# Kernel tuning notes

Measured on AMD Instinct MI355X. Metric: run time of the kernel, lower is better.

The kernel has to match this reference:

```python
import jax, jax.numpy as jnp
import numpy as np

NUM_GROUPS = 32
EPS = 1e-6
HEAD = 8


def group_norm(x, gamma, beta):
    # x: (b, c, h, w); normalize per group of channels over (c/g, h, w)
    b, c, h, w = x.shape
    g = NUM_GROUPS
    xg = x.reshape(b, g, c // g, h, w)
    mean = xg.mean(axis=(2, 3, 4), keepdims=True)
    var = xg.var(axis=(2, 3, 4), keepdims=True)
    xn = ((xg - mean) * jax.lax.rsqrt(var + EPS)).reshape(b, c, h, w)
    return xn * gamma[None, :, None, None] + beta[None, :, None, None]


def setup_inputs() -> dict:
    key = jax.random.key(0)
    ks = jax.random.split(key, 6)
    b, c, h, w = 8, 512, 64, 64
    sd = 1.0 / np.sqrt(c)
    return {
        "x": jax.random.normal(ks[0], (b, c, h, w), jnp.float32),
        "gamma": jnp.ones((c,), jnp.float32),
        "beta": jnp.zeros((c,), jnp.float32),
        "Wq": jax.random.normal(ks[1], (c, c), jnp.float32) * sd,
        "Wk": jax.random.normal(ks[2], (c, c), jnp.float32) * sd,
        "Wv": jax.random.normal(ks[3], (c, c), jnp.float32) * sd,
        "Wp": jax.random.normal(ks[4], (c, c), jnp.float32) * sd,
        "bp": jnp.zeros((c,), jnp.float32),
    }


def reference(x, gamma, beta, Wq, Wk, Wv, Wp, bp):
    b, c, h, w = x.shape
    hd = c // HEAD
    scale = jnp.sqrt(jnp.float32(hd))  # NOTE: original MULTIPLIES by sqrt(d)
    xn = group_norm(x, gamma, beta)            # (b, c, h, w)
    x_ = xn.reshape(b, c, h * w).transpose(0, 2, 1)  # (b, n, c), n = h*w
    # torch Linear: y = x @ W.T
    Q = (x_ @ Wq.T).reshape(b, h * w, HEAD, hd)
    K = (x_ @ Wk.T).reshape(b, h * w, HEAD, hd)
    V = (x_ @ Wv.T).reshape(b, h * w, HEAD, hd)
    # einsum 'bhid,bhjd->bhij' with axes (b, n, head, hd): per-position head gram
    dots = jnp.einsum('bnid,bnjd->bnij', Q, K) * scale  # (b, n, head, head)
    att = jax.nn.softmax(dots, axis=1)  # softmax over the SPATIAL axis (dim=1)
    out = jnp.einsum('bnij,bnjd->bnid', att, V).reshape(b, h * w, c)
    out = out @ Wp.T + bp  # dropout is identity at inference
    return out.transpose(0, 2, 1).reshape(b, c, h, w) + xn  # residual adds normed x
```

## Files before the change

kernel.cpp:

```cpp
#include <hip/hip_runtime.h>
#include <stdint.h>

typedef unsigned short ushort_t;
typedef _Float16 half8 __attribute__((ext_vector_type(8)));
typedef float f32x4 __attribute__((ext_vector_type(4)));

#define GLOBAL_AS __attribute__((address_space(1)))
#define LDS_AS    __attribute__((address_space(3)))

__device__ __forceinline__ float bf2f(ushort_t u) {
    union { unsigned i; float f; } v; v.i = ((unsigned)u) << 16; return v.f;
}
__device__ __forceinline__ ushort_t f2h(float f) {
    union { _Float16 h; ushort_t u; } v; v.h = (_Float16)f; return v.u;
}
__device__ __forceinline__ float h2f(ushort_t u) {
    union { _Float16 h; ushort_t u; } v; v.u = u; return (float)v.h;
}

__device__ __forceinline__ void async16(const void* g, void* l) {
    __builtin_amdgcn_global_load_lds((const GLOBAL_AS uint32_t*)g,
                                     (LDS_AS uint32_t*)l, 16, 0, 0);
}

__device__ __forceinline__ int is_bf16_in(const uint32_t* g32) {
    return *g32 == 0x3F803F80u;
}

__global__ __launch_bounds__(256) void prep(const void* Wq, const void* Wk,
                                            const void* Wv, const void* Wp,
                                            const void* g, const void* be, const void* bp,
                                            ushort_t* Wh, float* gcan, float* bcan,
                                            float* bpcan, const uint32_t* g32) {
    const int id = blockIdx.x;
    const int isbf = is_bf16_in(g32);
    if (id < 512) {
        const int wsel = id >> 7, wblk = id & 127;
        const void* src = (wsel == 0) ? Wq : (wsel == 1) ? Wk : (wsel == 2) ? Wv : Wp;
        ushort_t* dst = Wh + (size_t)wsel * 262144;
        const int e0 = wblk * 2048 + threadIdx.x * 8;
        ushort_t o[8];
        if (isbf) {
            uint4 u = *(const uint4*)((const ushort_t*)src + e0);
            const ushort_t* e = (const ushort_t*)&u;
#pragma unroll
            for (int j = 0; j < 8; ++j) o[j] = f2h(bf2f(e[j]));
        } else {
            float4 a = *(const float4*)((const float*)src + e0);
            float4 b = *(const float4*)((const float*)src + e0 + 4);
            o[0] = f2h(a.x); o[1] = f2h(a.y); o[2] = f2h(a.z); o[3] = f2h(a.w);
            o[4] = f2h(b.x); o[5] = f2h(b.y); o[6] = f2h(b.z); o[7] = f2h(b.w);
        }
        *(uint4*)(dst + e0) = *(const uint4*)o;
    } else {
        int t = threadIdx.x + (id - 512) * 256;
        if (isbf) {
            gcan[t]  = bf2f(((const ushort_t*)g)[t]);
            bcan[t]  = bf2f(((const ushort_t*)be)[t]);
            bpcan[t] = bf2f(((const ushort_t*)bp)[t]);
        } else {
            gcan[t]  = ((const float*)g)[t];
            bcan[t]  = ((const float*)be)[t];
            bpcan[t] = ((const float*)bp)[t];
        }
    }
}

__global__ __launch_bounds__(256) void gn_part(const void* xv, float* __restrict__ psums,
                                               const uint32_t* g32) {
    const int bx = blockIdx.x, t = threadIdx.x;
    const size_t base = (size_t)(bx >> 3) * 65536 + (size_t)(bx & 7) * 8192;
    float s = 0.f, sq = 0.f;
    if (is_bf16_in(g32)) {
        const ushort_t* p = (const ushort_t*)xv + base;
        for (int i = 0; i < 4; ++i) {
            uint4 u = ((const uint4*)p)[t + 256 * i];
            const ushort_t* e = (const ushort_t*)&u;
#pragma unroll
            for (int j = 0; j < 8; ++j) { float f = bf2f(e[j]); s += f; sq += f * f; }
        }
    } else {
        const float* p = (const float*)xv + base;
        for (int i = 0; i < 8; ++i) {
            float4 v = ((const float4*)p)[t + 256 * i];
            s += v.x + v.y + v.z + v.w;
            sq += v.x * v.x + v.y * v.y + v.z * v.z + v.w * v.w;
        }
    }
    __shared__ float ls[256], lq[256];
    ls[t] = s; lq[t] = sq;
    __syncthreads();
    for (int off = 128; off > 0; off >>= 1) {
        if (t < off) { ls[t] += ls[t + off]; lq[t] += lq[t + off]; }
        __syncthreads();
    }
    if (t == 0) { psums[bx * 2] = ls[0]; psums[bx * 2 + 1] = lq[0]; }
}

__global__ __launch_bounds__(256) void gn_apply_t(const void* xv,
                                                  const float* __restrict__ gcan,
                                                  const float* __restrict__ bcan,
                                                  const float* __restrict__ psums,
                                                  ushort_t* __restrict__ xnt,
                                                  ushort_t* __restrict__ xnc,
                                                  const uint32_t* g32) {
    const int nt = blockIdx.x;
    const int ct = blockIdx.y;
    const int b  = blockIdx.z;
    const int t  = threadIdx.x;
    const int c0 = ct * 64, n0 = nt * 64;
    __shared__ __align__(16) ushort_t tile[64 * 80];
    __shared__ float scS[64], shS[64];
    if (t < 64) {
        int c = c0 + t;
        int g = c >> 4;
        float s = 0.f, q = 0.f;
#pragma unroll
        for (int k = 0; k < 8; ++k) {
            s += psums[((b * 32 + g) * 8 + k) * 2];
            q += psums[((b * 32 + g) * 8 + k) * 2 + 1];
        }
        float mean = s * (1.f / 65536.f);
        float var  = q * (1.f / 65536.f) - mean * mean;
        float rstd = rsqrtf(fmaxf(var, 0.f) + 1e-6f);
        float sc = rstd * gcan[c];
        scS[t] = sc;
        shS[t] = bcan[c] - mean * sc;
    }
    __syncthreads();
    if (is_bf16_in(g32)) {
        const ushort_t* x = (const ushort_t*)xv;
#pragma unroll
        for (int p = 0; p < 2; ++p) {
            int u = p * 256 + t;
            int cc = u >> 3, nc = u & 7;
            int c = c0 + cc;
            size_t gidx = ((size_t)(b * 512 + c)) * 4096 + n0 + nc * 8;
            uint4 raw = *(const uint4*)(x + gidx);
            float sc = scS[cc], sh = shS[cc];
            const ushort_t* e = (const ushort_t*)&raw;
            ushort_t hv[8];
#pragma unroll
            for (int j = 0; j < 8; ++j) {
                hv[j] = f2h(bf2f(e[j]) * sc + sh);
                tile[(nc * 8 + j) * 80 + cc] = hv[j];
            }
            *(uint4*)(xnc + gidx) = *(const uint4*)hv;
        }
    } else {
        const float* x = (const float*)xv;
#pragma unroll
        for (int p = 0; p < 4; ++p) {
            int u = p * 256 + t;
            int cc = u >> 4, nc = u & 15;
            int c = c0 + cc;
            size_t gidx = ((size_t)(b * 512 + c)) * 4096 + n0 + nc * 4;
            float4 raw = *(const float4*)(x + gidx);
            float sc = scS[cc], sh = shS[cc];
            ushort_t hv[4];
            hv[0] = f2h(raw.x * sc + sh);
            hv[1] = f2h(raw.y * sc + sh);
            hv[2] = f2h(raw.z * sc + sh);
            hv[3] = f2h(raw.w * sc + sh);
#pragma unroll
            for (int j = 0; j < 4; ++j) tile[(nc * 4 + j) * 80 + cc] = hv[j];
            *(uint2*)(xnc + gidx) = *(const uint2*)hv;
        }
    }
    __syncthreads();
#pragma unroll
    for (int p = 0; p < 2; ++p) {
        int u = p * 256 + t;
        int nn = u >> 3, cchunk = u & 7;
        uint4 o = *(const uint4*)(tile + nn * 80 + cchunk * 8);
        *(uint4*)(xnt + ((size_t)(b * 4096 + n0 + nn)) * 512 + c0 + cchunk * 8) = o;
    }
}

__device__ __forceinline__ void gemm128_core(const ushort_t* __restrict__ A,
                                             const ushort_t* __restrict__ B,
                                             int m0, int n0, int K, f32x4 acc[4][4]) {
    __shared__ __align__(16) ushort_t As[128 * 32];
    __shared__ __align__(16) ushort_t Bs[128 * 32];
    const int t = threadIdx.x;
    const int l = t & 63;
    const int w = t >> 6;
    const int wm = (w >> 1) * 64, wn = (w & 1) * 64;
    const int lr = l & 15, q = l >> 4;
    f32x4 zero = {0.f, 0.f, 0.f, 0.f};
#pragma unroll
    for (int mi = 0; mi < 4; ++mi)
#pragma unroll
        for (int ni = 0; ni < 4; ++ni) acc[mi][ni] = zero;

    for (int kt = 0; kt < K; kt += 32) {
        __syncthreads();
#pragma unroll
        for (int p = 0; p < 2; ++p) {
            int s = p * 256 + t;
            int r = s >> 2, kc = s & 3;
            async16(A + (size_t)(m0 + r) * K + kt + kc * 8, (char*)As + p * 4096 + w * 1024);
            async16(B + (size_t)(n0 + r) * K + kt + kc * 8, (char*)Bs + p * 4096 + w * 1024);
        }
        __syncthreads();
        half8 af[4], bf[4];
#pragma unroll
        for (int mi = 0; mi < 4; ++mi)
            af[mi] = *(const half8*)(As + (wm + mi * 16 + lr) * 32 + q * 8);
#pragma unroll
        for (int ni = 0; ni < 4; ++ni)
            bf[ni] = *(const half8*)(Bs + (wn + ni * 16 + lr) * 32 + q * 8);
#pragma unroll
        for (int mi = 0; mi < 4; ++mi)
#pragma unroll
            for (int ni = 0; ni < 4; ++ni)
                acc[mi][ni] = __builtin_amdgcn_mfma_f32_16x16x32_f16(af[mi], bf[ni],
                                                                    acc[mi][ni], 0, 0, 0);
    }
}

__global__ __launch_bounds__(256) void gemm_qkv(const ushort_t* __restrict__ xnt,
                                                const ushort_t* __restrict__ Wh,
                                                ushort_t* __restrict__ Qo,
                                                ushort_t* __restrict__ Ko,
                                                ushort_t* __restrict__ Vo) {
    const int id = blockIdx.x;
    const int xcd = id & 7, s = id >> 3;
    const int mloc = s / 12, r = s % 12;
    const int m0 = (xcd * 32 + mloc) * 128;
    const int n0 = (r & 3) * 128;
    const int z  = r >> 2;
    const ushort_t* B = Wh + (size_t)z * 262144;
    ushort_t* C = (z == 0) ? Qo : (z == 1) ? Ko : Vo;
    f32x4 acc[4][4];
    gemm128_core(xnt, B, m0, n0, 512, acc);
    const int t = threadIdx.x, l = t & 63, w = t >> 6;
    const int wm = (w >> 1) * 64, wn = (w & 1) * 64;
    const int col = l & 15, q = l >> 4;
#pragma unroll
    for (int mi = 0; mi < 4; ++mi)
#pragma unroll
        for (int ni = 0; ni < 4; ++ni)
#pragma unroll
            for (int rr = 0; rr < 4; ++rr) {
                int row = wm + mi * 16 + q * 4 + rr;
                int cc  = wn + ni * 16 + col;
                C[(size_t)(m0 + row) * 512 + n0 + cc] = f2h(acc[mi][ni][rr]);
            }
}

__global__ __launch_bounds__(256) void dots_smax(const ushort_t* __restrict__ Q,
                                                 const ushort_t* __restrict__ K,
                                                 float* __restrict__ dots,
                                                 float* __restrict__ pmax,
                                                 float* __restrict__ psum) {
    const int chunk = blockIdx.x;
    const int t = threadIdx.x, l = t & 63, w = t >> 6;
    const int m = l & 15, q = l >> 4, col = m;
    __shared__ float sd[128][64];
    __shared__ float lm[4][64], lsum[4][64];
#pragma unroll
    for (int i = 0; i < 16; ++i) {
        int gpl = (i * 4 + w) * 2;
        int gp0 = chunk * 128 + gpl;
        const size_t base = (size_t)(gp0 + (m >> 3)) * 512 + (m & 7) * 64 + q * 8;
        half8 a0 = *(const half8*)(Q + base);
        half8 a1 = *(const half8*)(Q + base + 32);
        half8 b0 = *(const half8*)(K + base);
        half8 b1 = *(const half8*)(K + base + 32);
        f32x4 acc = {0.f, 0.f, 0.f, 0.f};
        acc = __builtin_amdgcn_mfma_f32_16x16x32_f16(a0, b0, acc, 0, 0, 0);
        acc = __builtin_amdgcn_mfma_f32_16x16x32_f16(a1, b1, acc, 0, 0, 0);
#pragma unroll
        for (int r = 0; r < 4; ++r) {
            int row = q * 4 + r;
            if (row < 8 && col < 8) {
                float v = acc[r] * 8.0f;
                int ij = row * 8 + col;
                sd[gpl][ij] = v;
                dots[(size_t)(gp0)*64 + ij] = v;
            }
            if (row >= 8 && col >= 8) {
                float v = acc[r] * 8.0f;
                int ij = (row - 8) * 8 + (col - 8);
                sd[gpl + 1][ij] = v;
                dots[(size_t)(gp0 + 1) * 64 + ij] = v;
            }
        }
    }
    __syncthreads();
    const int ij = l;
    float mx = -1e30f;
    float v[32];
#pragma unroll
    for (int r = 0; r < 32; ++r) { v[r] = sd[w * 32 + r][ij]; mx = fmaxf(mx, v[r]); }
    lm[w][ij] = mx;
    __syncthreads();
    float cm = fmaxf(fmaxf(lm[0][ij], lm[1][ij]), fmaxf(lm[2][ij], lm[3][ij]));
    float sum = 0.f;
#pragma unroll
    for (int r = 0; r < 32; ++r) sum += __expf(v[r] - cm);
    lsum[w][ij] = sum;
    __syncthreads();
    if (w == 0) {
        pmax[chunk * 64 + ij] = cm;
        psum[chunk * 64 + ij] = lsum[0][ij] + lsum[1][ij] + lsum[2][ij] + lsum[3][ij];
    }
}

__global__ __launch_bounds__(256) void attn_apply(const float* __restrict__ dots,
                                                  const float* __restrict__ pmax,
                                                  const float* __restrict__ psum,
                                                  const ushort_t* __restrict__ V,
                                                  ushort_t* __restrict__ P) {
    const int t = threadIdx.x, l = t & 63, w = t >> 6;
    const int gp_base = blockIdx.x * 16;
    const int b = gp_base >> 12;
    __shared__ float pm4[4][64], ps4[4][64];
    __shared__ float Mv[64], Siv[64];
    {
        const int cg = w * 8;
        float m = -1e30f;
        float pmv[8], psv[8];
#pragma unroll
        for (int c = 0; c < 8; ++c) {
            pmv[c] = pmax[(b * 32 + cg + c) * 64 + l];
            psv[c] = psum[(b * 32 + cg + c) * 64 + l];
            m = fmaxf(m, pmv[c]);
        }
        float s = 0.f;
#pragma unroll
        for (int c = 0; c < 8; ++c) s += psv[c] * __expf(pmv[c] - m);
        pm4[w][l] = m; ps4[w][l] = s;
    }
    __syncthreads();
    if (w == 0) {
        float M = fmaxf(fmaxf(pm4[0][l], pm4[1][l]), fmaxf(pm4[2][l], pm4[3][l]));
        float S = ps4[0][l] * __expf(pm4[0][l] - M) + ps4[1][l] * __expf(pm4[1][l] - M)
                + ps4[2][l] * __expf(pm4[2][l] - M) + ps4[3][l] * __expf(pm4[3][l] - M);
        Mv[l] = M;
        Siv[l] = 1.f / S;
    }
    __syncthreads();
    const float mv = Mv[l], siv = Siv[l];
    __shared__ float att[4][64];
    __shared__ __align__(16) ushort_t vb[4][512];
    const int i = l >> 3, dc = l & 7;
    for (int p = 0; p < 4; ++p) {
        int gp = gp_base + w * 4 + p;
        float d = dots[(size_t)gp * 64 + l];
        att[w][l] = __expf(d - mv) * siv;
        *(uint4*)(&vb[w][l * 8]) = *(const uint4*)(V + (size_t)gp * 512 + l * 8);
        __syncthreads();
        float o[8] = {0, 0, 0, 0, 0, 0, 0, 0};
#pragma unroll
        for (int j = 0; j < 8; ++j) {
            float a = att[w][i * 8 + j];
            uint4 vv = *(const uint4*)(&vb[w][j * 64 + dc * 8]);
            const ushort_t* ve = (const ushort_t*)&vv;
#pragma unroll
            for (int k2 = 0; k2 < 8; ++k2) o[k2] += a * h2f(ve[k2]);
        }
        ushort_t ou[8];
#pragma unroll
        for (int k2 = 0; k2 < 8; ++k2) ou[k2] = f2h(o[k2]);
        *(uint4*)(P + (size_t)gp * 512 + l * 8) = *(const uint4*)ou;
        __syncthreads();
    }
}

__global__ __launch_bounds__(256) void gemm_out(const ushort_t* __restrict__ Wph,
                                                const ushort_t* __restrict__ P,
                                                const ushort_t* __restrict__ xnc,
                                                const float* __restrict__ bpcan,
                                                float* __restrict__ out) {
    const int id = blockIdx.x;
    const int xcd = id & 7, s = id >> 3;
    const int pair = xcd * 32 + (s >> 2);
    const int o0 = (s & 3) * 128;
    const int b  = pair >> 5;
    const int n0 = (pair & 31) * 128;
    f32x4 acc[4][4];
    gemm128_core(Wph, P + (size_t)b * 4096 * 512, o0, n0, 512, acc);
    const int t = threadIdx.x, l = t & 63, w = t >> 6;
    const int wm = (w >> 1) * 64, wn = (w & 1) * 64;
    const int col = l & 15, q = l >> 4;
#pragma unroll
    for (int mi = 0; mi < 4; ++mi) {
#pragma unroll
        for (int r = 0; r < 4; ++r) {
            int o = o0 + wm + mi * 16 + q * 4 + r;
            float bias = bpcan[o];
#pragma unroll
            for (int ni = 0; ni < 4; ++ni) {
                int n = n0 + wn + ni * 16 + col;
                size_t idx = ((size_t)(b * 512 + o)) * 4096 + n;
                out[idx] = acc[mi][ni][r] + bias + h2f(xnc[idx]);
            }
        }
    }
}

extern "C" void kernel_launch(void* const* d_in, const int* in_sizes, int n_in,
                              void* d_out, int out_size, void* d_ws, size_t ws_size,
                              hipStream_t stream) {
    const void* x     = d_in[0];
    const void* gamma = d_in[1];
    const void* beta  = d_in[2];
    const void* Wq    = d_in[3];
    const void* Wk    = d_in[4];
    const void* Wv    = d_in[5];
    const void* Wp    = d_in[6];
    const void* bp    = d_in[7];
    const uint32_t* g32 = (const uint32_t*)gamma;
    float* out = (float*)d_out;

    char* ws = (char*)d_ws;
    const size_t SZ = 33554432;
    ushort_t* xnt = (ushort_t*)(ws);
    ushort_t* Qh  = (ushort_t*)(ws + 1 * SZ);
    ushort_t* Kh  = (ushort_t*)(ws + 2 * SZ);
    ushort_t* Vh  = (ushort_t*)(ws + 3 * SZ);
    float* dots   = (float*)(ws + 4 * SZ);
    ushort_t* Wh  = (ushort_t*)(ws + 4 * SZ + 8388608);
    ushort_t* xnc = (ushort_t*)(ws + 4 * SZ + 8388608 + 2097152);
    char* tail    = ws + 4 * SZ + 8388608 + 2097152 + SZ;
    float* gcan   = (float*)(tail);
    float* bcan   = gcan + 512;
    float* bpcan  = bcan + 512;
    float* psums  = bpcan + 512;
    float* pmax   = psums + 4096;
    float* psumS  = pmax + 16384;
    ushort_t* Pb  = xnt;

    prep      <<<514, 256, 0, stream>>>(Wq, Wk, Wv, Wp, gamma, beta, bp,
                                        Wh, gcan, bcan, bpcan, g32);
    gn_part   <<<2048, 256, 0, stream>>>(x, psums, g32);
    gn_apply_t<<<dim3(64, 8, 8), 256, 0, stream>>>(x, gcan, bcan, psums, xnt, xnc, g32);
    gemm_qkv  <<<3072, 256, 0, stream>>>(xnt, Wh, Qh, Kh, Vh);
    dots_smax <<<256, 256, 0, stream>>>(Qh, Kh, dots, pmax, psumS);
    attn_apply<<<2048, 256, 0, stream>>>(dots, pmax, psumS, Vh, Pb);
    gemm_out  <<<1024, 256, 0, stream>>>(Wh + 3 * 262144, Pb, xnc, bpcan, out);
}
```

Measured before the change: 288.2 us.

## Double-buffer GEMM LDS tiles with XOR swizzle and drop per-wave barriers

```diff
diff --git a/kernel.cpp b/kernel.cpp
--- a/kernel.cpp
+++ b/kernel.cpp
@@ -177,46 +177,69 @@
     }
 }
 
+__device__ __forceinline__ void mfma_tile(const ushort_t* Ab, const ushort_t* Bb,
+                                          int wm, int wn, int lr, int qe,
+                                          f32x4 acc[4][4]) {
+    half8 af[4], bf[4];
+#pragma unroll
+    for (int mi = 0; mi < 4; ++mi)
+        af[mi] = *(const half8*)(Ab + (wm + mi * 16 + lr) * 32 + qe * 8);
+#pragma unroll
+    for (int ni = 0; ni < 4; ++ni)
+        bf[ni] = *(const half8*)(Bb + (wn + ni * 16 + lr) * 32 + qe * 8);
+#pragma unroll
+    for (int mi = 0; mi < 4; ++mi)
+#pragma unroll
+        for (int ni = 0; ni < 4; ++ni)
+            acc[mi][ni] = __builtin_amdgcn_mfma_f32_16x16x32_f16(af[mi], bf[ni],
+                                                                 acc[mi][ni], 0, 0, 0);
+}
+
 __device__ __forceinline__ void gemm128_core(const ushort_t* __restrict__ A,
                                              const ushort_t* __restrict__ B,
                                              int m0, int n0, int K, f32x4 acc[4][4]) {
-    __shared__ __align__(16) ushort_t As[128 * 32];
-    __shared__ __align__(16) ushort_t Bs[128 * 32];
+    __shared__ __align__(16) ushort_t As[2][128 * 32];
+    __shared__ __align__(16) ushort_t Bs[2][128 * 32];
     const int t = threadIdx.x;
     const int l = t & 63;
     const int w = t >> 6;
     const int wm = (w >> 1) * 64, wn = (w & 1) * 64;
     const int lr = l & 15, q = l >> 4;
+    const int qe = q ^ ((lr >> 1) & 3);
+    const int r0 = t >> 2;
+    const int kc = (t & 3) ^ ((r0 >> 1) & 3);
+    const ushort_t* gA0 = A + (size_t)(m0 + r0) * K + kc * 8;
+    const ushort_t* gB0 = B + (size_t)(n0 + r0) * K + kc * 8;
+    const ushort_t* gA1 = gA0 + (size_t)64 * K;
+    const ushort_t* gB1 = gB0 + (size_t)64 * K;
+
     f32x4 zero = {0.f, 0.f, 0.f, 0.f};
 #pragma unroll
     for (int mi = 0; mi < 4; ++mi)
 #pragma unroll
         for (int ni = 0; ni < 4; ++ni) acc[mi][ni] = zero;
 
-    for (int kt = 0; kt < K; kt += 32) {
-        __syncthreads();
-#pragma unroll
-        for (int p = 0; p < 2; ++p) {
-            int s = p * 256 + t;
-            int r = s >> 2, kc = s & 3;
-            async16(A + (size_t)(m0 + r) * K + kt + kc * 8, (char*)As + p * 4096 + w * 1024);
-            async16(B + (size_t)(n0 + r) * K + kt + kc * 8, (char*)Bs + p * 4096 + w * 1024);
-        }
-        __syncthreads();
-        half8 af[4], bf[4];
-#pragma unroll
-        for (int mi = 0; mi < 4; ++mi)
-            af[mi] = *(const half8*)(As + (wm + mi * 16 + lr) * 32 + q * 8);
-#pragma unroll
-        for (int ni = 0; ni < 4; ++ni)
-            bf[ni] = *(const half8*)(Bs + (wn + ni * 16 + lr) * 32 + q * 8);
-#pragma unroll
-        for (int mi = 0; mi < 4; ++mi)
-#pragma unroll
-            for (int ni = 0; ni < 4; ++ni)
-                acc[mi][ni] = __builtin_amdgcn_mfma_f32_16x16x32_f16(af[mi], bf[ni],
-                                                                    acc[mi][ni], 0, 0, 0);
-    }
+    {
+        char* sA = (char*)&As[0][0] + w * 1024;
+        char* sB = (char*)&Bs[0][0] + w * 1024;
+        async16(gA0, sA); async16(gA1, sA + 4096);
+        async16(gB0, sB); async16(gB1, sB + 4096);
+    }
+    asm volatile("s_waitcnt vmcnt(0)" ::: "memory");
+    __builtin_amdgcn_s_barrier();
+
+    int cur = 0;
+    for (int kt = 32; kt < K; kt += 32) {
+        char* sA = (char*)&As[cur ^ 1][0] + w * 1024;
+        char* sB = (char*)&Bs[cur ^ 1][0] + w * 1024;
+        async16(gA0 + kt, sA); async16(gA1 + kt, sA + 4096);
+        async16(gB0 + kt, sB); async16(gB1 + kt, sB + 4096);
+        mfma_tile(&As[cur][0], &Bs[cur][0], wm, wn, lr, qe, acc);
+        asm volatile("s_waitcnt vmcnt(0)" ::: "memory");
+        __builtin_amdgcn_s_barrier();
+        cur ^= 1;
+    }
+    mfma_tile(&As[cur][0], &Bs[cur][0], wm, wn, lr, qe, acc);
 }
 
 __global__ __launch_bounds__(256) void gemm_qkv(const ushort_t* __restrict__ xnt,
@@ -351,7 +374,6 @@
         float d = dots[(size_t)gp * 64 + l];
         att[w][l] = __expf(d - mv) * siv;
         *(uint4*)(&vb[w][l * 8]) = *(const uint4*)(V + (size_t)gp * 512 + l * 8);
-        __syncthreads();
         float o[8] = {0, 0, 0, 0, 0, 0, 0, 0};
 #pragma unroll
         for (int j = 0; j < 8; ++j) {
@@ -365,7 +387,6 @@
 #pragma unroll
         for (int k2 = 0; k2 < 8; ++k2) ou[k2] = f2h(o[k2]);
         *(uint4*)(P + (size_t)gp * 512 + l * 8) = *(const uint4*)ou;
-        __syncthreads();
     }
 }
 
```

After: 309.2 us. 7.3% more time.

## Replace 128-tile GEMM core with double-buffered swizzled 256x256 tile pipeline

Applied to the files above, without the earlier changes.

```diff
diff --git a/kernel.cpp b/kernel.cpp
--- a/kernel.cpp
+++ b/kernel.cpp
@@ -177,75 +177,112 @@
     }
 }
 
-__device__ __forceinline__ void gemm128_core(const ushort_t* __restrict__ A,
-                                             const ushort_t* __restrict__ B,
-                                             int m0, int n0, int K, f32x4 acc[4][4]) {
-    __shared__ __align__(16) ushort_t As[128 * 32];
-    __shared__ __align__(16) ushort_t Bs[128 * 32];
+__device__ __forceinline__ void gemm256_core(const ushort_t* __restrict__ A,
+                                             const ushort_t* __restrict__ Bm,
+                                             int m0, int n0, f32x4 acc[8][4]) {
+    __shared__ __align__(16) ushort_t lds[2][4][8192];
     const int t = threadIdx.x;
-    const int l = t & 63;
-    const int w = t >> 6;
-    const int wm = (w >> 1) * 64, wn = (w & 1) * 64;
+    const int l = t & 63, w = t >> 6;
+    const int wmi = w >> 2, wni = w & 3;
     const int lr = l & 15, q = l >> 4;
+    const int rxor = lr & 7;
+    const int sr = t >> 3;
+    const int sc = (t & 7) ^ (sr & 7);
+
     f32x4 zero = {0.f, 0.f, 0.f, 0.f};
 #pragma unroll
-    for (int mi = 0; mi < 4; ++mi)
-#pragma unroll
-        for (int ni = 0; ni < 4; ++ni) acc[mi][ni] = zero;
-
-    for (int kt = 0; kt < K; kt += 32) {
-        __syncthreads();
-#pragma unroll
-        for (int p = 0; p < 2; ++p) {
-            int s = p * 256 + t;
-            int r = s >> 2, kc = s & 3;
-            async16(A + (size_t)(m0 + r) * K + kt + kc * 8, (char*)As + p * 4096 + w * 1024);
-            async16(B + (size_t)(n0 + r) * K + kt + kc * 8, (char*)Bs + p * 4096 + w * 1024);
-        }
-        __syncthreads();
-        half8 af[4], bf[4];
-#pragma unroll
-        for (int mi = 0; mi < 4; ++mi)
-            af[mi] = *(const half8*)(As + (wm + mi * 16 + lr) * 32 + q * 8);
-#pragma unroll
-        for (int ni = 0; ni < 4; ++ni)
-            bf[ni] = *(const half8*)(Bs + (wn + ni * 16 + lr) * 32 + q * 8);
-#pragma unroll
-        for (int mi = 0; mi < 4; ++mi)
-#pragma unroll
-            for (int ni = 0; ni < 4; ++ni)
-                acc[mi][ni] = __builtin_amdgcn_mfma_f32_16x16x32_f16(af[mi], bf[ni],
-                                                                    acc[mi][ni], 0, 0, 0);
-    }
-}
-
-__global__ __launch_bounds__(256) void gemm_qkv(const ushort_t* __restrict__ xnt,
-                                                const ushort_t* __restrict__ Wh,
-                                                ushort_t* __restrict__ Qo,
-                                                ushort_t* __restrict__ Ko,
-                                                ushort_t* __restrict__ Vo) {
+    for (int mf = 0; mf < 8; ++mf)
+#pragma unroll
+        for (int nf = 0; nf < 4; ++nf) acc[mf][nf] = zero;
+
+    auto stage = [&](int kt, int h) {
+        const ushort_t* src = ((h < 2) ? A + (size_t)(m0 + h * 128 + sr) * 512
+                                       : Bm + (size_t)(n0 + (h - 2) * 128 + sr) * 512)
+                              + kt * 64 + sc * 8;
+        ushort_t* dst = &lds[kt & 1][h][w * 512];
+        async16(src, dst);
+        async16(src + 64 * 512, dst + 4096);
+    };
+
+    stage(0, 0); stage(0, 1); stage(0, 2); stage(0, 3);
+    stage(1, 2); stage(1, 3);
+    asm volatile("s_waitcnt vmcnt(4)" ::: "memory");
+    __builtin_amdgcn_s_barrier();
+
+    half8 bfr[4][2];
+    for (int kt = 0; kt < 8; ++kt) {
+        const ushort_t* Ah = &lds[kt & 1][wmi][0];
+        const ushort_t* Bh = &lds[kt & 1][2 + (wni >> 1)][(wni & 1) * 4096];
+#pragma unroll
+        for (int p = 0; p < 4; ++p) {
+            half8 afr[2][2];
+#pragma unroll
+            for (int i = 0; i < 2; ++i)
+#pragma unroll
+                for (int kh = 0; kh < 2; ++kh)
+                    afr[i][kh] = *(const half8*)(Ah + (2 * p + i) * 1024 + lr * 64 +
+                                                 (((kh << 2) | q) ^ rxor) * 8);
+            if (p == 0) {
+#pragma unroll
+                for (int nf = 0; nf < 4; ++nf)
+#pragma unroll
+                    for (int kh = 0; kh < 2; ++kh)
+                        bfr[nf][kh] = *(const half8*)(Bh + nf * 1024 + lr * 64 +
+                                                      (((kh << 2) | q) ^ rxor) * 8);
+            }
+            if (p < 2) { if (kt + 1 < 8) stage(kt + 1, p); }
+            else       { if (kt + 2 < 8) stage(kt + 2, p); }
+            __builtin_amdgcn_s_barrier();
+            asm volatile("s_waitcnt lgkmcnt(0)" ::: "memory");
+            __builtin_amdgcn_sched_barrier(0);
+            __builtin_amdgcn_s_setprio(1);
+#pragma unroll
+            for (int i = 0; i < 2; ++i)
+#pragma unroll
+                for (int nf = 0; nf < 4; ++nf) {
+                    acc[2 * p + i][nf] = __builtin_amdgcn_mfma_f32_16x16x32_f16(
+                        afr[i][0], bfr[nf][0], acc[2 * p + i][nf], 0, 0, 0);
+                    acc[2 * p + i][nf] = __builtin_amdgcn_mfma_f32_16x16x32_f16(
+                        afr[i][1], bfr[nf][1], acc[2 * p + i][nf], 0, 0, 0);
+                }
+            __builtin_amdgcn_s_setprio(0);
+            __builtin_amdgcn_s_barrier();
+        }
+        if (kt < 7) {
+            if (kt < 6) asm volatile("s_waitcnt vmcnt(4)" ::: "memory");
+            else        asm volatile("s_waitcnt vmcnt(0)" ::: "memory");
+            __builtin_amdgcn_s_barrier();
+        }
+    }
+}
+
+__global__ __launch_bounds__(512, 2) void gemm_qkv(const ushort_t* __restrict__ xnt,
+                                                   const ushort_t* __restrict__ Wh,
+                                                   ushort_t* __restrict__ Qo,
+                                                   ushort_t* __restrict__ Ko,
+                                                   ushort_t* __restrict__ Vo) {
     const int id = blockIdx.x;
     const int xcd = id & 7, s = id >> 3;
-    const int mloc = s / 12, r = s % 12;
-    const int m0 = (xcd * 32 + mloc) * 128;
-    const int n0 = (r & 3) * 128;
-    const int z  = r >> 2;
+    const int mloc = s / 6, r = s % 6;
+    const int m0 = (xcd * 16 + mloc) * 256;
+    const int n0 = (r & 1) * 256;
+    const int z  = r >> 1;
     const ushort_t* B = Wh + (size_t)z * 262144;
     ushort_t* C = (z == 0) ? Qo : (z == 1) ? Ko : Vo;
-    f32x4 acc[4][4];
-    gemm128_core(xnt, B, m0, n0, 512, acc);
+    f32x4 acc[8][4];
+    gemm256_core(xnt, B, m0, n0, acc);
     const int t = threadIdx.x, l = t & 63, w = t >> 6;
-    const int wm = (w >> 1) * 64, wn = (w & 1) * 64;
-    const int col = l & 15, q = l >> 4;
-#pragma unroll
-    for (int mi = 0; mi < 4; ++mi)
-#pragma unroll
-        for (int ni = 0; ni < 4; ++ni)
+    const int wmi = w >> 2, wni = w & 3;
+    const int lr = l & 15, q = l >> 4;
+#pragma unroll
+    for (int mf = 0; mf < 8; ++mf)
+#pragma unroll
+        for (int nf = 0; nf < 4; ++nf)
 #pragma unroll
             for (int rr = 0; rr < 4; ++rr) {
-                int row = wm + mi * 16 + q * 4 + rr;
-                int cc  = wn + ni * 16 + col;
-                C[(size_t)(m0 + row) * 512 + n0 + cc] = f2h(acc[mi][ni][rr]);
+                int row = m0 + wmi * 128 + mf * 16 + q * 4 + rr;
+                int cc  = n0 + wni * 64 + nf * 16 + lr;
+                C[(size_t)row * 512 + cc] = f2h(acc[mf][nf][rr]);
             }
 }
 
@@ -351,7 +388,6 @@
         float d = dots[(size_t)gp * 64 + l];
         att[w][l] = __expf(d - mv) * siv;
         *(uint4*)(&vb[w][l * 8]) = *(const uint4*)(V + (size_t)gp * 512 + l * 8);
-        __syncthreads();
         float o[8] = {0, 0, 0, 0, 0, 0, 0, 0};
 #pragma unroll
         for (int j = 0; j < 8; ++j) {
@@ -365,37 +401,35 @@
 #pragma unroll
         for (int k2 = 0; k2 < 8; ++k2) ou[k2] = f2h(o[k2]);
         *(uint4*)(P + (size_t)gp * 512 + l * 8) = *(const uint4*)ou;
-        __syncthreads();
-    }
-}
-
-__global__ __launch_bounds__(256) void gemm_out(const ushort_t* __restrict__ Wph,
-                                                const ushort_t* __restrict__ P,
-                                                const ushort_t* __restrict__ xnc,
-                                                const float* __restrict__ bpcan,
-                                                float* __restrict__ out) {
+    }
+}
+
+__global__ __launch_bounds__(512, 2) void gemm_out(const ushort_t* __restrict__ Wph,
+                                                   const ushort_t* __restrict__ P,
+                                                   const ushort_t* __restrict__ xnc,
+                                                   const float* __restrict__ bpcan,
+                                                   float* __restrict__ out) {
     const int id = blockIdx.x;
-    const int xcd = id & 7, s = id >> 3;
-    const int pair = xcd * 32 + (s >> 2);
-    const int o0 = (s & 3) * 128;
-    const int b  = pair >> 5;
-    const int n0 = (pair & 31) * 128;
-    f32x4 acc[4][4];
-    gemm128_core(Wph, P + (size_t)b * 4096 * 512, o0, n0, 512, acc);
+    const int b  = id & 7;
+    const int s  = id >> 3;
+    const int o0 = (s & 1) * 256;
+    const int n1 = (s >> 1) * 256;
+    f32x4 acc[8][4];
+    gemm256_core(Wph, P + (size_t)b * 4096 * 512, o0, n1, acc);
     const int t = threadIdx.x, l = t & 63, w = t >> 6;
-    const int wm = (w >> 1) * 64, wn = (w & 1) * 64;
-    const int col = l & 15, q = l >> 4;
-#pragma unroll
-    for (int mi = 0; mi < 4; ++mi) {
-#pragma unroll
-        for (int r = 0; r < 4; ++r) {
-            int o = o0 + wm + mi * 16 + q * 4 + r;
+    const int wmi = w >> 2, wni = w & 3;
+    const int lr = l & 15, q = l >> 4;
+#pragma unroll
+    for (int mf = 0; mf < 8; ++mf) {
+#pragma unroll
+        for (int rr = 0; rr < 4; ++rr) {
+            int o = o0 + wmi * 128 + mf * 16 + q * 4 + rr;
             float bias = bpcan[o];
 #pragma unroll
-            for (int ni = 0; ni < 4; ++ni) {
-                int n = n0 + wn + ni * 16 + col;
+            for (int nf = 0; nf < 4; ++nf) {
+                int n = n1 + wni * 64 + nf * 16 + lr;
                 size_t idx = ((size_t)(b * 512 + o)) * 4096 + n;
-                out[idx] = acc[mi][ni][r] + bias + h2f(xnc[idx]);
+                out[idx] = acc[mf][nf][rr] + bias + h2f(xnc[idx]);
             }
         }
     }
@@ -437,8 +471,8 @@
                                         Wh, gcan, bcan, bpcan, g32);
     gn_part   <<<2048, 256, 0, stream>>>(x, psums, g32);
     gn_apply_t<<<dim3(64, 8, 8), 256, 0, stream>>>(x, gcan, bcan, psums, xnt, xnc, g32);
-    gemm_qkv  <<<3072, 256, 0, stream>>>(xnt, Wh, Qh, Kh, Vh);
+    gemm_qkv  <<<768, 512, 0, stream>>>(xnt, Wh, Qh, Kh, Vh);
     dots_smax <<<256, 256, 0, stream>>>(Qh, Kh, dots, pmax, psumS);
     attn_apply<<<2048, 256, 0, stream>>>(dots, pmax, psumS, Vh, Pb);
-    gemm_out  <<<1024, 256, 0, stream>>>(Wh + 3 * 262144, Pb, xnc, bpcan, out);
-}
+    gemm_out  <<<256, 512, 0, stream>>>(Wh + 3 * 262144, Pb, xnc, bpcan, out);
+}
```

Result: faster. 267.8 us (-7.1%).
